# Performance work log

Hardware: AMD Instinct MI355X
Metric: run time of the kernel (lower is better)

The kernel has to match this reference:

```python
import jax, jax.numpy as jnp
import numpy as np

B, S, EMBED, HEADS = 2, 2048, 2048, 16
HEAD_DIM = EMBED // HEADS  # 128


def setup_inputs() -> dict:
    key = jax.random.key(0)
    k1, k2, k3 = jax.random.split(key, 3)
    x = jax.random.normal(k1, (B, S, EMBED), dtype=jnp.float32)
    # qkv_proj: Linear(EMBED -> 3*EMBED, bias=False); stored as [in, out]
    w_qkv = jax.random.normal(k2, (EMBED, 3 * EMBED), dtype=jnp.float32) / np.float32(np.sqrt(EMBED))
    # out_proj: Linear(EMBED -> EMBED, bias=False)
    w_out = jax.random.normal(k3, (EMBED, EMBED), dtype=jnp.float32) / np.float32(np.sqrt(EMBED))
    return {"x": x, "w_qkv": w_qkv, "w_out": w_out}


def reference(x, w_qkv, w_out):
    b, s, e = x.shape
    h, d = HEADS, e // HEADS
    qkv = x @ w_qkv                                  # [b, s, 3e]
    q, k, v = jnp.split(qkv, 3, axis=-1)             # each [b, s, e]
    q = q.reshape(b, s, h, d).transpose(0, 2, 1, 3)  # [b, h, s, d]
    k = k.reshape(b, s, h, d).transpose(0, 2, 1, 3)
    v = v.reshape(b, s, h, d).transpose(0, 2, 1, 3)
    scale = jnp.asarray(1.0 / np.sqrt(d), dtype=q.dtype)
    scores = jnp.einsum('bhqd,bhkd->bhqk', q, k) * scale  # [b, h, s, s]
    causal = jnp.tril(jnp.ones((s, s), dtype=bool))
    scores = jnp.where(causal, scores, -jnp.inf)
    attn = jax.nn.softmax(scores, axis=-1)
    ctx = jnp.einsum('bhqk,bhkd->bhqd', attn, v)     # [b, h, s, d]
    ctx = ctx.transpose(0, 2, 1, 3).reshape(b, s, e)
    return ctx @ w_out
```

## Files before the change

### kernel.cpp

```cpp
#include <hip/hip_runtime.h>
#include <cstdint>

#define S_LEN 2048
#define EMB   2048
#define NHEAD 16
#define HDIM  128
#define MROWS 4096
#define NQKV  6144

typedef __bf16 bf16x8 __attribute__((ext_vector_type(8)));
typedef __bf16 bf16x4 __attribute__((ext_vector_type(4)));
typedef float  f32x4  __attribute__((ext_vector_type(4)));

#define MFMA16(a, b, c) __builtin_amdgcn_mfma_f32_16x16x32_bf16((a), (b), (c), 0, 0, 0)

__device__ __forceinline__ unsigned short f2bf(float f) {
  unsigned u = __builtin_bit_cast(unsigned, f);
  u += 0x7fffu + ((u >> 16) & 1u);
  return (unsigned short)(u >> 16);
}
__device__ __forceinline__ float bf2f(unsigned short u) {
  unsigned v = ((unsigned)u) << 16;
  return __builtin_bit_cast(float, v);
}

__device__ __forceinline__ void gl_lds16(const unsigned short* g, unsigned short* l) {
  __builtin_amdgcn_global_load_lds(
      (const __attribute__((address_space(1))) void*)(uintptr_t)g,
      (__attribute__((address_space(3))) void*)(unsigned int)(uintptr_t)l,
      16, 0, 0);
}

__global__ void cast_bf16(const float* __restrict__ in, unsigned short* __restrict__ out, int n) {
  int i = (blockIdx.x * 256 + threadIdx.x) * 4;
  if (i >= n) return;
  float4 v = *(const float4*)(in + i);
  ushort4 o;
  o.x = f2bf(v.x); o.y = f2bf(v.y); o.z = f2bf(v.z); o.w = f2bf(v.w);
  *(ushort4*)(out + i) = o;
}

__global__ void transpose_cast(const float* __restrict__ in, unsigned short* __restrict__ out,
                               int R, int C) {
  __shared__ float tile[32][33];
  int bx = blockIdx.x << 5;
  int by = blockIdx.y << 5;
  int tx = threadIdx.x, ty = threadIdx.y;
  for (int j = 0; j < 32; j += 8)
    tile[ty + j][tx] = in[(size_t)(by + ty + j) * C + bx + tx];
  __syncthreads();
  for (int j = 0; j < 32; j += 8)
    out[(size_t)(bx + ty + j) * R + by + tx] = f2bf(tile[tx][ty + j]);
}

__global__ __launch_bounds__(512, 2) void gemm_qkv8(const unsigned short* __restrict__ A,
                                                    const unsigned short* __restrict__ Bt,
                                                    unsigned short* __restrict__ Qo,
                                                    unsigned short* __restrict__ Ko,
                                                    unsigned short* __restrict__ Vt) {
  extern __shared__ unsigned short lds[];
  unsigned short* Abuf = lds;
  unsigned short* Bbuf = lds + 32768;

  const int tid = threadIdx.x, w = tid >> 6, lane = tid & 63;
  const int fr = lane & 15, g = lane >> 4;
  const int gm = w >> 2, gn = w & 3;
  const int srow = tid >> 3, jp = tid & 7;

  const int bid = blockIdx.x;
  const int wg = (bid & 7) * 64 + (bid >> 3);
  const int mt = wg >> 5, nt = wg & 31;
  const int m0 = mt << 8;
  const int n0 = nt * 192;

  auto issueB = [&](int buf, int kk, int third) {
    const int row = (third << 6) + srow;
    gl_lds16(Bt + (size_t)(n0 + row) * 2048 + kk + ((jp ^ (row & 7)) << 3),
             Bbuf + buf * 12288 + (row << 6) + (jp << 3));
  };
  auto issueA = [&](int buf, int kk, int q) {
    const int row = (q << 6) + srow;
    gl_lds16(A + (size_t)(m0 + row) * 2048 + kk + ((jp ^ (row & 7)) << 3),
             Abuf + buf * 16384 + (row << 6) + (jp << 3));
  };

  f32x4 acc[8][3] = {};
  bf16x8 alo[4][2], ahi[4][2], bv[2][2], bc2[2];

  issueB(0, 0, 0); issueB(0, 0, 1); issueB(0, 0, 2);
  issueA(0, 0, 0); issueA(0, 0, 1); issueA(0, 0, 2); issueA(0, 0, 3);

  for (int t = 0; t < 32; ++t) {
    const int cb = t & 1, nb = cb ^ 1;
    const unsigned short* Ab = Abuf + cb * 16384;
    const unsigned short* Bb = Bbuf + cb * 12288;
    const int kn = (t + 1) << 6;

    asm volatile("s_waitcnt vmcnt(2)" ::: "memory");
    asm volatile("" ::: "memory");
    __builtin_amdgcn_s_barrier();
    asm volatile("" ::: "memory");
    if (t < 31) { issueB(nb, kn, 0); issueB(nb, kn, 1); issueB(nb, kn, 2); }
#pragma unroll
    for (int r = 0; r < 4; ++r)
#pragma unroll
      for (int ks = 0; ks < 2; ++ks)
        alo[r][ks] = *(const bf16x8*)(Ab + ((gm * 64 + r * 16 + fr) << 6) +
                                      ((((ks << 2) + g) ^ (fr & 7)) << 3));
#pragma unroll
    for (int c = 0; c < 2; ++c)
#pragma unroll
      for (int ks = 0; ks < 2; ++ks)
        bv[c][ks] = *(const bf16x8*)(Bb + ((gn * 48 + c * 16 + fr) << 6) +
                                     ((((ks << 2) + g) ^ (fr & 7)) << 3));
    __builtin_amdgcn_s_setprio(1);
#pragma unroll
    for (int ks = 0; ks < 2; ++ks)
#pragma unroll
      for (int r = 0; r < 4; ++r)
#pragma unroll
        for (int c = 0; c < 2; ++c)
          acc[r][c] = MFMA16(alo[r][ks], bv[c][ks], acc[r][c]);
    __builtin_amdgcn_s_setprio(0);

    if (t < 31) { asm volatile("s_waitcnt vmcnt(3)" ::: "memory"); }
    else        { asm volatile("s_waitcnt vmcnt(0)" ::: "memory"); }
    asm volatile("" ::: "memory");
    __builtin_amdgcn_s_barrier();
    asm volatile("" ::: "memory");
    if (t < 31) { issueA(nb, kn, 0); issueA(nb, kn, 1); }
#pragma unroll
    for (int ks = 0; ks < 2; ++ks)
      bc2[ks] = *(const bf16x8*)(Bb + ((gn * 48 + 32 + fr) << 6) +
                                 ((((ks << 2) + g) ^ (fr & 7)) << 3));
    __builtin_amdgcn_s_setprio(1);
#pragma unroll
    for (int ks = 0; ks < 2; ++ks)
#pragma unroll
      for (int r = 0; r < 4; ++r)
        acc[r][2] = MFMA16(alo[r][ks], bc2[ks], acc[r][2]);
    __builtin_amdgcn_s_setprio(0);
#pragma unroll
    for (int r = 0; r < 4; ++r)
#pragma unroll
      for (int ks = 0; ks < 2; ++ks)
        ahi[r][ks] = *(const bf16x8*)(Ab + ((128 + gm * 64 + r * 16 + fr) << 6) +
                                      ((((ks << 2) + g) ^ (fr & 7)) << 3));
    __builtin_amdgcn_s_setprio(1);
#pragma unroll
    for (int ks = 0; ks < 2; ++ks)
#pragma unroll
      for (int r = 0; r < 4; ++r)
        acc[4 + r][2] = MFMA16(ahi[r][ks], bc2[ks], acc[4 + r][2]);
    __builtin_amdgcn_s_setprio(0);

    asm volatile("" ::: "memory");
    __builtin_amdgcn_s_barrier();
    asm volatile("" ::: "memory");
    if (t < 31) { issueA(nb, kn, 2); issueA(nb, kn, 3); }
#pragma unroll
    for (int c = 0; c < 2; ++c)
#pragma unroll
      for (int ks = 0; ks < 2; ++ks)
        bv[c][ks] = *(const bf16x8*)(Bb + ((gn * 48 + c * 16 + fr) << 6) +
                                     ((((ks << 2) + g) ^ (fr & 7)) << 3));
    __builtin_amdgcn_s_setprio(1);
#pragma unroll
    for (int ks = 0; ks < 2; ++ks)
#pragma unroll
      for (int r = 0; r < 4; ++r)
#pragma unroll
        for (int c = 0; c < 2; ++c)
          acc[4 + r][c] = MFMA16(ahi[r][ks], bv[c][ks], acc[4 + r][c]);
    __builtin_amdgcn_s_setprio(0);
  }

  const int rowb = m0 & (S_LEN - 1);
  const int bbase = (m0 >> 11) * NHEAD;
  for (int r = 0; r < 8; ++r) {
    const int sl = rowb + ((r >> 2) << 7) + (gm << 6) + ((r & 3) << 4) + (g << 2);
    for (int c = 0; c < 3; ++c) {
      const int ncol = n0 + gn * 48 + c * 16;
      const int which = ncol >> 11;
      const int h = (ncol >> 7) & 15;
      const int d = (ncol & 127) + fr;
      const int bh = bbase + h;
      if (which == 2) {
        ushort4 pk;
        pk.x = f2bf(acc[r][c][0]); pk.y = f2bf(acc[r][c][1]);
        pk.z = f2bf(acc[r][c][2]); pk.w = f2bf(acc[r][c][3]);
        *(ushort4*)(Vt + ((size_t)bh * HDIM + d) * S_LEN + sl) = pk;
      } else {
        unsigned short* dst = which ? Ko : Qo;
        for (int q4 = 0; q4 < 4; ++q4)
          dst[((size_t)bh * S_LEN + sl + q4) * HDIM + d] = f2bf(acc[r][c][q4]);
      }
    }
  }
}

__global__ __launch_bounds__(256, 3) void attn(const unsigned short* __restrict__ Qg,
                                               const unsigned short* __restrict__ Kg,
                                               const unsigned short* __restrict__ Vtg,
                                               unsigned short* __restrict__ ctx,
                                               unsigned short* __restrict__ Opart,
                                               float* __restrict__ Lp) {
  __shared__ __align__(16) unsigned short SA[16384];
  __shared__ __align__(16) unsigned short Ps[8192];
  unsigned short* Qs = SA;
  unsigned short* Ks = SA;
  unsigned short* Vs = SA + 8192;

  const int blk = blockIdx.x;
  const int bh = blk & 31;
  const int t = blk >> 5;
  int qt, kt0, nkt, part;
  if (t < 8)       { qt = t;     kt0 = 0;  nkt = 2 * t + 2;       part = -1; }
  else if (t < 16) { qt = t;     kt0 = 0;  nkt = 16;              part = (bh << 3) + (qt - 8); }
  else             { qt = t - 8; kt0 = 16; nkt = 2 * qt - 14;     part = 256 + (bh << 3) + (qt - 8); }

  const int tid = threadIdx.x, wave = tid >> 6, lane = tid & 63;
  const int fr = lane & 15, g = lane >> 4;

  const unsigned short* qsrc = Qg + ((size_t)bh * S_LEN + (qt << 7)) * HDIM;
  for (int i = 0; i < 8; ++i) {
    int s0 = (i * 256 + tid) << 3;
    int q = s0 >> 7, jp = (s0 >> 3) & 15;
    gl_lds16(qsrc + (q << 7) + ((jp ^ (q & 15)) << 3), Qs + s0);
  }
  __builtin_amdgcn_s_waitcnt(0);
  __syncthreads();

  bf16x8 qf[2][4];
  for (int nbq = 0; nbq < 2; ++nbq)
    for (int kd = 0; kd < 4; ++kd) {
      int q = (wave << 5) + (nbq << 4) + fr;
      qf[nbq][kd] = *(const bf16x8*)(Qs + (q << 7) + ((((kd << 2) + g) ^ fr) << 3));
    }
  __syncthreads();

  float lsum[2] = {0.f, 0.f};
  f32x4 oacc[2][8] = {};
  const float scale = 0.08838834764831845f;

  const unsigned short* kbase = Kg + (size_t)bh * S_LEN * HDIM;
  const unsigned short* vbase = Vtg + (size_t)bh * HDIM * S_LEN;

  for (int kti = 0; kti < nkt; ++kti) {
    const int kt = kt0 + kti;
    const unsigned short* ks = kbase + ((size_t)kt << 6) * HDIM;
    const unsigned short* vs = vbase + (kt << 6);
    for (int i = 0; i < 4; ++i) {
      int s0 = (i * 256 + tid) << 3;
      int key = s0 >> 7, jk = (s0 >> 3) & 15;
      gl_lds16(ks + (key << 7) + ((jk ^ (key & 15)) << 3), Ks + s0);
      int d = s0 >> 6, jv = (s0 >> 3) & 7;
      gl_lds16(vs + (size_t)d * S_LEN + ((jv ^ (d & 7)) << 3), Vs + s0);
    }
    __builtin_amdgcn_s_waitcnt(0);
    __syncthreads();

    f32x4 sacc[2][4] = {};
    for (int kd = 0; kd < 4; ++kd)
      for (int kb = 0; kb < 4; ++kb) {
        bf16x8 kf = *(const bf16x8*)(Ks + (((kb << 4) + fr) << 7) + ((((kd << 2) + g) ^ fr) << 3));
        sacc[0][kb] = MFMA16(kf, qf[0][kd], sacc[0][kb]);
        sacc[1][kb] = MFMA16(kf, qf[1][kd], sacc[1][kb]);
      }

    const bool diag = (kt >= 2 * qt);
    for (int nbq = 0; nbq < 2; ++nbq) {
      const int qg = (qt << 7) + (wave << 5) + (nbq << 4) + fr;
      float sum = 0.f;
      for (int kb = 0; kb < 4; ++kb) {
        float p[4];
        for (int r = 0; r < 4; ++r) {
          float v = sacc[nbq][kb][r] * scale;
          if (diag) {
            int keyg = (kt << 6) + (kb << 4) + (g << 2) + r;
            if (keyg > qg) v = -__builtin_inff();
          }
          p[r] = __expf(v);
          sum += p[r];
        }
        ushort4 pk;
        pk.x = f2bf(p[0]); pk.y = f2bf(p[1]);
        pk.z = f2bf(p[2]); pk.w = f2bf(p[3]);
        *(ushort4*)(Ps + (((wave << 3) + (nbq << 2) + kb) << 8) + (lane << 2)) = pk;
      }
      lsum[nbq] += sum;
    }

    __builtin_amdgcn_s_waitcnt(0);

    for (int kc = 0; kc < 2; ++kc) {
      const int kbr = (kc << 1) + (g >> 1);
      bf16x8 ap[2];
      for (int h2 = 0; h2 < 2; ++h2) {
        const unsigned short* pb =
            Ps + (((wave << 3) + (h2 << 2) + kbr) << 8) + ((g & 1) << 7) + (fr << 2);
        bf16x4 a0 = *(const bf16x4*)pb;
        bf16x4 a1 = *(const bf16x4*)(pb + 64);
        bf16x8 a;
        a[0] = a0[0]; a[1] = a0[1]; a[2] = a0[2]; a[3] = a0[3];
        a[4] = a1[0]; a[5] = a1[1]; a[6] = a1[2]; a[7] = a1[3];
        ap[h2] = a;
      }
      for (int nd = 0; nd < 8; ++nd) {
        bf16x8 bv = *(const bf16x8*)(Vs + (((nd << 4) + fr) << 6) + ((((kc << 2) + g) ^ (fr & 7)) << 3));
        oacc[0][nd] = MFMA16(ap[0], bv, oacc[0][nd]);
        oacc[1][nd] = MFMA16(ap[1], bv, oacc[1][nd]);
      }
    }
    __syncthreads();
  }

  for (int nbq = 0; nbq < 2; ++nbq) {
    lsum[nbq] += __shfl_xor(lsum[nbq], 16);
    lsum[nbq] += __shfl_xor(lsum[nbq], 32);
  }

  if (part < 0) {
    const int b = bh >> 4, h = bh & 15;
    for (int mq = 0; mq < 2; ++mq)
      for (int r = 0; r < 4; ++r) {
        float lv = __shfl(lsum[mq], (lane & 48) | ((g << 2) + r));
        const float il = 1.0f / lv;
        const int s = (qt << 7) + (wave << 5) + (mq << 4) + (g << 2) + r;
        unsigned short* dst = ctx + ((size_t)(b * S_LEN + s) * EMB) + (h << 7);
        for (int nd = 0; nd < 8; ++nd)
          dst[(nd << 4) + fr] = f2bf(oacc[mq][nd][r] * il);
      }
  } else {
    unsigned short* Ob = Opart + ((size_t)part << 14);
    for (int mq = 0; mq < 2; ++mq)
      for (int r = 0; r < 4; ++r) {
        const int ql = (wave << 5) + (mq << 4) + (g << 2) + r;
        unsigned short* dst = Ob + (ql << 7);
        for (int nd = 0; nd < 8; ++nd)
          dst[(nd << 4) + fr] = f2bf(oacc[mq][nd][r]);
      }
    if (g == 0)
      for (int nbq = 0; nbq < 2; ++nbq) {
        const int ql = (wave << 5) + (nbq << 4) + fr;
        Lp[(part << 7) + ql] = lsum[nbq];
      }
  }
}

__global__ void attn_combine(const unsigned short* __restrict__ Op,
                             const float* __restrict__ Lp,
                             unsigned short* __restrict__ ctx) {
  const int tid = threadIdx.x;
  const int rid = blockIdx.x * 16 + (tid >> 4);
  const int l16 = tid & 15;
  const int bh = rid >> 10;
  const int qtl = (rid >> 7) & 7;
  const int ql = rid & 127;
  const int p = (bh << 3) + qtl;
  const float lA = Lp[(p << 7) + ql];
  const float lB = Lp[((256 + p) << 7) + ql];
  const float il = 1.0f / (lA + lB);
  const int d0 = l16 << 3;
  const unsigned short* a = Op + ((size_t)p << 14) + (ql << 7) + d0;
  const unsigned short* b = Op + ((size_t)(256 + p) << 14) + (ql << 7) + d0;
  const int bb = bh >> 4, h = bh & 15;
  const int s = ((qtl + 8) << 7) + ql;
  unsigned short* dst = ctx + ((size_t)(bb * S_LEN + s) * EMB) + (h << 7) + d0;
  ushort4 va0 = *(const ushort4*)a, va1 = *(const ushort4*)(a + 4);
  ushort4 vb0 = *(const ushort4*)b, vb1 = *(const ushort4*)(b + 4);
  ushort4 o0, o1;
  o0.x = f2bf((bf2f(va0.x) + bf2f(vb0.x)) * il);
  o0.y = f2bf((bf2f(va0.y) + bf2f(vb0.y)) * il);
  o0.z = f2bf((bf2f(va0.z) + bf2f(vb0.z)) * il);
  o0.w = f2bf((bf2f(va0.w) + bf2f(vb0.w)) * il);
  o1.x = f2bf((bf2f(va1.x) + bf2f(vb1.x)) * il);
  o1.y = f2bf((bf2f(va1.y) + bf2f(vb1.y)) * il);
  o1.z = f2bf((bf2f(va1.z) + bf2f(vb1.z)) * il);
  o1.w = f2bf((bf2f(va1.w) + bf2f(vb1.w)) * il);
  *(ushort4*)dst = o0;
  *(ushort4*)(dst + 4) = o1;
}

__global__ __launch_bounds__(256, 3) void gemm_out(const unsigned short* __restrict__ A,
                                                   const unsigned short* __restrict__ Bt,
                                                   float* __restrict__ C) {
  __shared__ __align__(16) unsigned short As[128 * 64];
  __shared__ __align__(16) unsigned short Bs[128 * 64];
  const int tid = threadIdx.x;
  const int n0 = blockIdx.x << 7;
  const int m0 = blockIdx.y << 7;
  const int wave = tid >> 6, lane = tid & 63;
  const int wm = (wave & 1) << 6, wn = (wave >> 1) << 6;
  const int fr = lane & 15, g = lane >> 4;
  const int q = tid >> 3;
  const int jp = tid & 7;
  f32x4 acc[4][4] = {};
  for (int k0 = 0; k0 < 2048; k0 += 64) {
    for (int i = 0; i < 4; ++i) {
      const int row = q + (i << 5);
      const int jsw = (jp ^ (row & 7)) << 3;
      gl_lds16(A + (size_t)(m0 + row) * 2048 + k0 + jsw, As + (row << 6) + (jp << 3));
      gl_lds16(Bt + (size_t)(n0 + row) * 2048 + k0 + jsw, Bs + (row << 6) + (jp << 3));
    }
    __builtin_amdgcn_s_waitcnt(0);
    __syncthreads();
    for (int ks = 0; ks < 2; ++ks) {
      const int slot = (((ks << 2) + g) ^ (fr & 7)) << 3;
      bf16x8 af[4], bfv[4];
      for (int i = 0; i < 4; ++i) af[i]  = *(const bf16x8*)(As + ((wm + (i << 4) + fr) << 6) + slot);
      for (int j = 0; j < 4; ++j) bfv[j] = *(const bf16x8*)(Bs + ((wn + (j << 4) + fr) << 6) + slot);
      for (int i = 0; i < 4; ++i)
        for (int j = 0; j < 4; ++j)
          acc[i][j] = MFMA16(af[i], bfv[j], acc[i][j]);
    }
    __syncthreads();
  }
  for (int i = 0; i < 4; ++i) {
    const int row = m0 + wm + (i << 4) + (g << 2);
    for (int j = 0; j < 4; ++j) {
      const int col = n0 + wn + (j << 4) + fr;
      for (int r = 0; r < 4; ++r)
        C[(size_t)(row + r) * EMB + col] = acc[i][j][r];
    }
  }
}

extern "C" void kernel_launch(void* const* d_in, const int* in_sizes, int n_in,
                              void* d_out, int out_size, void* d_ws, size_t ws_size,
                              hipStream_t stream) {
  const float* x    = (const float*)d_in[0];
  const float* wqkv = (const float*)d_in[1];
  const float* wout = (const float*)d_in[2];
  float* out = (float*)d_out;

  unsigned short* ws = (unsigned short*)d_ws;
  const size_t NELEM = (size_t)MROWS * EMB;
  unsigned short* xb    = ws;
  unsigned short* wqkvT = xb + NELEM;
  unsigned short* woutT = wqkvT + (size_t)NQKV * EMB;
  unsigned short* Q     = woutT + (size_t)EMB * EMB;
  unsigned short* K     = Q + NELEM;
  unsigned short* Vt    = K + NELEM;
  unsigned short* ctx   = xb;
  unsigned short* Opart = wqkvT;
  float* Lp = (float*)(Opart + ((size_t)512 << 14));

  static bool attr_done = false;
  if (!attr_done) {
    (void)hipFuncSetAttribute((const void*)gemm_qkv8,
                              hipFuncAttributeMaxDynamicSharedMemorySize, 114688);
    attr_done = true;
  }

  cast_bf16<<<8192, 256, 0, stream>>>(x, xb, (int)NELEM);
  transpose_cast<<<dim3(NQKV / 32, EMB / 32), dim3(32, 8), 0, stream>>>(wqkv, wqkvT, EMB, NQKV);
  transpose_cast<<<dim3(EMB / 32, EMB / 32), dim3(32, 8), 0, stream>>>(wout, woutT, EMB, EMB);
  gemm_qkv8<<<512, 512, 114688, stream>>>(xb, wqkvT, Q, K, Vt);
  attn<<<768, 256, 0, stream>>>(Q, K, Vt, ctx, Opart, Lp);
  attn_combine<<<2048, 256, 0, stream>>>(Opart, Lp, ctx);
  gemm_out<<<dim3(EMB / 128, MROWS / 128), 256, 0, stream>>>(ctx, woutT, out);
}
```

Measured before the change: 365.1 us.

## Share a templated pipelined GEMM core between the QKV and output projections

```diff
diff --git a/kernel.cpp b/kernel.cpp
--- a/kernel.cpp
+++ b/kernel.cpp
@@ -30,6 +30,9 @@
       (__attribute__((address_space(3))) void*)(unsigned int)(uintptr_t)l,
       16, 0, 0);
 }
+
+#define FENCE() asm volatile("" ::: "memory")
+#define BARRIER() do { FENCE(); __builtin_amdgcn_s_barrier(); FENCE(); } while (0)
 
 __global__ void cast_bf16(const float* __restrict__ in, unsigned short* __restrict__ out, int n) {
   int i = (blockIdx.x * 256 + threadIdx.x) * 4;
@@ -53,134 +56,160 @@
     out[(size_t)(bx + ty + j) * R + by + tx] = f2bf(tile[tx][ty + j]);
 }
 
-__global__ __launch_bounds__(512, 2) void gemm_qkv8(const unsigned short* __restrict__ A,
+template<int NCOL>
+__device__ __forceinline__ void gemm_pipe2(const unsigned short* __restrict__ Ap,
+                                           const unsigned short* __restrict__ Bp,
+                                           int m0, int n0, f32x4 (&acc)[8][NCOL]) {
+  constexpr int BN = 128 * NCOL;
+  constexpr int BISS = 2 * NCOL;
+  constexpr int NT = 32;
+  extern __shared__ unsigned short lds[];
+  unsigned short* Abuf = lds;
+  unsigned short* Bbuf = lds + 16384;
+
+  const int tid = threadIdx.x, w = tid >> 6, lane = tid & 63;
+  const int fr = lane & 15, g = lane >> 4;
+  const int srow = tid >> 3, jp = tid & 7;
+
+  auto issueA = [&](int buf, int kk, int idx) {
+    const int row = (idx << 6) + srow;
+    gl_lds16(Ap + (size_t)(m0 + row) * 2048 + kk + ((jp ^ (row & 7)) << 3),
+             Abuf + (buf << 13) + (row << 6) + (jp << 3));
+  };
+  auto issueB = [&](int buf, int kk, int idx) {
+    const int row = (idx << 6) + srow;
+    gl_lds16(Bp + (size_t)(n0 + row) * 2048 + kk + ((jp ^ (row & 7)) << 3),
+             Bbuf + buf * (BN * 64) + (row << 6) + (jp << 3));
+  };
+
+#pragma unroll
+  for (int i = 0; i < BISS; ++i) issueB(0, 0, i);
+  issueA(0, 0, 0); issueA(0, 0, 1);
+  issueB(1, 64, 0); issueB(1, 64, 1);
+  asm volatile("s_waitcnt vmcnt(2)" ::: "memory");
+  __builtin_amdgcn_s_barrier();
+  FENCE();
+
+  bf16x8 bfr[NCOL][2];
+  for (int t = 0; t < NT; ++t) {
+    const int cb = t & 1, nb = cb ^ 1;
+    const unsigned short* Ab = Abuf + (cb << 13);
+    const unsigned short* Bb = Bbuf + cb * (BN * 64);
+    const int kn = (t + 1) << 6;
+    const bool s1 = (t + 1 < NT), s2 = (t + 2 < NT);
+
+    bf16x8 af[2][2];
+#pragma unroll
+    for (int c = 0; c < NCOL; ++c)
+#pragma unroll
+      for (int ks = 0; ks < 2; ++ks)
+        bfr[c][ks] = *(const bf16x8*)(Bb + ((w * 16 * NCOL + c * 16 + fr) << 6) +
+                                      ((((ks << 2) + g) ^ (fr & 7)) << 3));
+#pragma unroll
+    for (int rr = 0; rr < 2; ++rr)
+#pragma unroll
+      for (int ks = 0; ks < 2; ++ks)
+        af[rr][ks] = *(const bf16x8*)(Ab + (((rr * 16) + fr) << 6) +
+                                      ((((ks << 2) + g) ^ (fr & 7)) << 3));
+    if (s1) {
+      issueB(nb, kn, 2); issueB(nb, kn, 3);
+      if (NCOL == 3) issueB(nb, kn, 4);
+    }
+    BARRIER();
+    __builtin_amdgcn_s_setprio(1);
+#pragma unroll
+    for (int ks = 0; ks < 2; ++ks)
+#pragma unroll
+      for (int rr = 0; rr < 2; ++rr)
+#pragma unroll
+        for (int c = 0; c < NCOL; ++c)
+          acc[rr][c] = MFMA16(af[rr][ks], bfr[c][ks], acc[rr][c]);
+    __builtin_amdgcn_s_setprio(0);
+
+#pragma unroll
+    for (int rr = 0; rr < 2; ++rr)
+#pragma unroll
+      for (int ks = 0; ks < 2; ++ks)
+        af[rr][ks] = *(const bf16x8*)(Ab + (((32 + rr * 16) + fr) << 6) +
+                                      ((((ks << 2) + g) ^ (fr & 7)) << 3));
+    if (s1) {
+      if (NCOL == 3) issueB(nb, kn, 5);
+      issueA(nb, kn, 0); issueA(nb, kn, 1);
+    }
+    BARRIER();
+    __builtin_amdgcn_s_setprio(1);
+#pragma unroll
+    for (int ks = 0; ks < 2; ++ks)
+#pragma unroll
+      for (int rr = 0; rr < 2; ++rr)
+#pragma unroll
+        for (int c = 0; c < NCOL; ++c)
+          acc[2 + rr][c] = MFMA16(af[rr][ks], bfr[c][ks], acc[2 + rr][c]);
+    __builtin_amdgcn_s_setprio(0);
+
+#pragma unroll
+    for (int rr = 0; rr < 2; ++rr)
+#pragma unroll
+      for (int ks = 0; ks < 2; ++ks)
+        af[rr][ks] = *(const bf16x8*)(Ab + (((64 + rr * 16) + fr) << 6) +
+                                      ((((ks << 2) + g) ^ (fr & 7)) << 3));
+    BARRIER();
+    __builtin_amdgcn_s_setprio(1);
+#pragma unroll
+    for (int ks = 0; ks < 2; ++ks)
+#pragma unroll
+      for (int rr = 0; rr < 2; ++rr)
+#pragma unroll
+        for (int c = 0; c < NCOL; ++c)
+          acc[4 + rr][c] = MFMA16(af[rr][ks], bfr[c][ks], acc[4 + rr][c]);
+    __builtin_amdgcn_s_setprio(0);
+
+#pragma unroll
+    for (int rr = 0; rr < 2; ++rr)
+#pragma unroll
+      for (int ks = 0; ks < 2; ++ks)
+        af[rr][ks] = *(const bf16x8*)(Ab + (((96 + rr * 16) + fr) << 6) +
+                                      ((((ks << 2) + g) ^ (fr & 7)) << 3));
+    if (s2) {
+      const int kn2 = (t + 2) << 6;
+      issueB(cb, kn2, 0); issueB(cb, kn2, 1);
+      asm volatile("s_waitcnt vmcnt(2)" ::: "memory");
+    } else if (s1) {
+      asm volatile("s_waitcnt vmcnt(0)" ::: "memory");
+    }
+    BARRIER();
+    __builtin_amdgcn_s_setprio(1);
+#pragma unroll
+    for (int ks = 0; ks < 2; ++ks)
+#pragma unroll
+      for (int rr = 0; rr < 2; ++rr)
+#pragma unroll
+        for (int c = 0; c < NCOL; ++c)
+          acc[6 + rr][c] = MFMA16(af[rr][ks], bfr[c][ks], acc[6 + rr][c]);
+    __builtin_amdgcn_s_setprio(0);
+  }
+}
+
+__global__ __launch_bounds__(512, 2) void gemm_qkv9(const unsigned short* __restrict__ A,
                                                     const unsigned short* __restrict__ Bt,
                                                     unsigned short* __restrict__ Qo,
                                                     unsigned short* __restrict__ Ko,
                                                     unsigned short* __restrict__ Vt) {
-  extern __shared__ unsigned short lds[];
-  unsigned short* Abuf = lds;
-  unsigned short* Bbuf = lds + 32768;
+  const int bid = blockIdx.x;
+  const int wg = (bid & 7) * 64 + (bid >> 3);
+  const int mt = wg & 31, nt = wg >> 5;
+  const int m0 = mt << 7, n0 = nt * 384;
+  f32x4 acc[8][3] = {};
+  gemm_pipe2<3>(A, Bt, m0, n0, acc);
 
   const int tid = threadIdx.x, w = tid >> 6, lane = tid & 63;
   const int fr = lane & 15, g = lane >> 4;
-  const int gm = w >> 2, gn = w & 3;
-  const int srow = tid >> 3, jp = tid & 7;
-
-  const int bid = blockIdx.x;
-  const int wg = (bid & 7) * 64 + (bid >> 3);
-  const int mt = wg >> 5, nt = wg & 31;
-  const int m0 = mt << 8;
-  const int n0 = nt * 192;
-
-  auto issueB = [&](int buf, int kk, int third) {
-    const int row = (third << 6) + srow;
-    gl_lds16(Bt + (size_t)(n0 + row) * 2048 + kk + ((jp ^ (row & 7)) << 3),
-             Bbuf + buf * 12288 + (row << 6) + (jp << 3));
-  };
-  auto issueA = [&](int buf, int kk, int q) {
-    const int row = (q << 6) + srow;
-    gl_lds16(A + (size_t)(m0 + row) * 2048 + kk + ((jp ^ (row & 7)) << 3),
-             Abuf + buf * 16384 + (row << 6) + (jp << 3));
-  };
-
-  f32x4 acc[8][3] = {};
-  bf16x8 alo[4][2], ahi[4][2], bv[2][2], bc2[2];
-
-  issueB(0, 0, 0); issueB(0, 0, 1); issueB(0, 0, 2);
-  issueA(0, 0, 0); issueA(0, 0, 1); issueA(0, 0, 2); issueA(0, 0, 3);
-
-  for (int t = 0; t < 32; ++t) {
-    const int cb = t & 1, nb = cb ^ 1;
-    const unsigned short* Ab = Abuf + cb * 16384;
-    const unsigned short* Bb = Bbuf + cb * 12288;
-    const int kn = (t + 1) << 6;
-
-    asm volatile("s_waitcnt vmcnt(2)" ::: "memory");
-    asm volatile("" ::: "memory");
-    __builtin_amdgcn_s_barrier();
-    asm volatile("" ::: "memory");
-    if (t < 31) { issueB(nb, kn, 0); issueB(nb, kn, 1); issueB(nb, kn, 2); }
-#pragma unroll
-    for (int r = 0; r < 4; ++r)
-#pragma unroll
-      for (int ks = 0; ks < 2; ++ks)
-        alo[r][ks] = *(const bf16x8*)(Ab + ((gm * 64 + r * 16 + fr) << 6) +
-                                      ((((ks << 2) + g) ^ (fr & 7)) << 3));
-#pragma unroll
-    for (int c = 0; c < 2; ++c)
-#pragma unroll
-      for (int ks = 0; ks < 2; ++ks)
-        bv[c][ks] = *(const bf16x8*)(Bb + ((gn * 48 + c * 16 + fr) << 6) +
-                                     ((((ks << 2) + g) ^ (fr & 7)) << 3));
-    __builtin_amdgcn_s_setprio(1);
-#pragma unroll
-    for (int ks = 0; ks < 2; ++ks)
-#pragma unroll
-      for (int r = 0; r < 4; ++r)
-#pragma unroll
-        for (int c = 0; c < 2; ++c)
-          acc[r][c] = MFMA16(alo[r][ks], bv[c][ks], acc[r][c]);
-    __builtin_amdgcn_s_setprio(0);
-
-    if (t < 31) { asm volatile("s_waitcnt vmcnt(3)" ::: "memory"); }
-    else        { asm volatile("s_waitcnt vmcnt(0)" ::: "memory"); }
-    asm volatile("" ::: "memory");
-    __builtin_amdgcn_s_barrier();
-    asm volatile("" ::: "memory");
-    if (t < 31) { issueA(nb, kn, 0); issueA(nb, kn, 1); }
-#pragma unroll
-    for (int ks = 0; ks < 2; ++ks)
-      bc2[ks] = *(const bf16x8*)(Bb + ((gn * 48 + 32 + fr) << 6) +
-                                 ((((ks << 2) + g) ^ (fr & 7)) << 3));
-    __builtin_amdgcn_s_setprio(1);
-#pragma unroll
-    for (int ks = 0; ks < 2; ++ks)
-#pragma unroll
-      for (int r = 0; r < 4; ++r)
-        acc[r][2] = MFMA16(alo[r][ks], bc2[ks], acc[r][2]);
-    __builtin_amdgcn_s_setprio(0);
-#pragma unroll
-    for (int r = 0; r < 4; ++r)
-#pragma unroll
-      for (int ks = 0; ks < 2; ++ks)
-        ahi[r][ks] = *(const bf16x8*)(Ab + ((128 + gm * 64 + r * 16 + fr) << 6) +
-                                      ((((ks << 2) + g) ^ (fr & 7)) << 3));
-    __builtin_amdgcn_s_setprio(1);
-#pragma unroll
-    for (int ks = 0; ks < 2; ++ks)
-#pragma unroll
-      for (int r = 0; r < 4; ++r)
-        acc[4 + r][2] = MFMA16(ahi[r][ks], bc2[ks], acc[4 + r][2]);
-    __builtin_amdgcn_s_setprio(0);
-
-    asm volatile("" ::: "memory");
-    __builtin_amdgcn_s_barrier();
-    asm volatile("" ::: "memory");
-    if (t < 31) { issueA(nb, kn, 2); issueA(nb, kn, 3); }
-#pragma unroll
-    for (int c = 0; c < 2; ++c)
-#pragma unroll
-      for (int ks = 0; ks < 2; ++ks)
-        bv[c][ks] = *(const bf16x8*)(Bb + ((gn * 48 + c * 16 + fr) << 6) +
-                                     ((((ks << 2) + g) ^ (fr & 7)) << 3));
-    __builtin_amdgcn_s_setprio(1);
-#pragma unroll
-    for (int ks = 0; ks < 2; ++ks)
-#pragma unroll
-      for (int r = 0; r < 4; ++r)
-#pragma unroll
-        for (int c = 0; c < 2; ++c)
-          acc[4 + r][c] = MFMA16(ahi[r][ks], bv[c][ks], acc[4 + r][c]);
-    __builtin_amdgcn_s_setprio(0);
-  }
-
   const int rowb = m0 & (S_LEN - 1);
   const int bbase = (m0 >> 11) * NHEAD;
   for (int r = 0; r < 8; ++r) {
-    const int sl = rowb + ((r >> 2) << 7) + (gm << 6) + ((r & 3) << 4) + (g << 2);
+    const int sl = rowb + r * 16 + (g << 2);
     for (int c = 0; c < 3; ++c) {
-      const int ncol = n0 + gn * 48 + c * 16;
+      const int ncol = n0 + w * 48 + c * 16;
       const int which = ncol >> 11;
       const int h = (ncol >> 7) & 15;
       const int d = (ncol & 127) + fr;
@@ -195,6 +224,28 @@
         for (int q4 = 0; q4 < 4; ++q4)
           dst[((size_t)bh * S_LEN + sl + q4) * HDIM + d] = f2bf(acc[r][c][q4]);
       }
+    }
+  }
+}
+
+__global__ __launch_bounds__(512, 2) void gemm_out9(const unsigned short* __restrict__ A,
+                                                    const unsigned short* __restrict__ Bt,
+                                                    float* __restrict__ C) {
+  const int bid = blockIdx.x;
+  const int wg = (bid & 7) * 32 + (bid >> 3);
+  const int mt = wg & 31, nt = wg >> 5;
+  const int m0 = mt << 7, n0 = nt << 8;
+  f32x4 acc[8][2] = {};
+  gemm_pipe2<2>(A, Bt, m0, n0, acc);
+
+  const int tid = threadIdx.x, w = tid >> 6, lane = tid & 63;
+  const int fr = lane & 15, g = lane >> 4;
+  for (int r = 0; r < 8; ++r) {
+    const int row = m0 + r * 16 + (g << 2);
+    for (int c = 0; c < 2; ++c) {
+      const int col = n0 + w * 32 + c * 16 + fr;
+      for (int q4 = 0; q4 < 4; ++q4)
+        C[(size_t)(row + q4) * EMB + col] = acc[r][c][q4];
     }
   }
 }
@@ -382,50 +433,6 @@
   *(ushort4*)(dst + 4) = o1;
 }
 
-__global__ __launch_bounds__(256, 3) void gemm_out(const unsigned short* __restrict__ A,
-                                                   const unsigned short* __restrict__ Bt,
-                                                   float* __restrict__ C) {
-  __shared__ __align__(16) unsigned short As[128 * 64];
-  __shared__ __align__(16) unsigned short Bs[128 * 64];
-  const int tid = threadIdx.x;
-  const int n0 = blockIdx.x << 7;
-  const int m0 = blockIdx.y << 7;
-  const int wave = tid >> 6, lane = tid & 63;
-  const int wm = (wave & 1) << 6, wn = (wave >> 1) << 6;
-  const int fr = lane & 15, g = lane >> 4;
-  const int q = tid >> 3;
-  const int jp = tid & 7;
-  f32x4 acc[4][4] = {};
-  for (int k0 = 0; k0 < 2048; k0 += 64) {
-    for (int i = 0; i < 4; ++i) {
-      const int row = q + (i << 5);
-      const int jsw = (jp ^ (row & 7)) << 3;
-      gl_lds16(A + (size_t)(m0 + row) * 2048 + k0 + jsw, As + (row << 6) + (jp << 3));
-      gl_lds16(Bt + (size_t)(n0 + row) * 2048 + k0 + jsw, Bs + (row << 6) + (jp << 3));
-    }
-    __builtin_amdgcn_s_waitcnt(0);
-    __syncthreads();
-    for (int ks = 0; ks < 2; ++ks) {
-      const int slot = (((ks << 2) + g) ^ (fr & 7)) << 3;
-      bf16x8 af[4], bfv[4];
-      for (int i = 0; i < 4; ++i) af[i]  = *(const bf16x8*)(As + ((wm + (i << 4) + fr) << 6) + slot);
-      for (int j = 0; j < 4; ++j) bfv[j] = *(const bf16x8*)(Bs + ((wn + (j << 4) + fr) << 6) + slot);
-      for (int i = 0; i < 4; ++i)
-        for (int j = 0; j < 4; ++j)
-          acc[i][j] = MFMA16(af[i], bfv[j], acc[i][j]);
-    }
-    __syncthreads();
-  }
-  for (int i = 0; i < 4; ++i) {
-    const int row = m0 + wm + (i << 4) + (g << 2);
-    for (int j = 0; j < 4; ++j) {
-      const int col = n0 + wn + (j << 4) + fr;
-      for (int r = 0; r < 4; ++r)
-        C[(size_t)(row + r) * EMB + col] = acc[i][j][r];
-    }
-  }
-}
-
 extern "C" void kernel_launch(void* const* d_in, const int* in_sizes, int n_in,
                               void* d_out, int out_size, void* d_ws, size_t ws_size,
                               hipStream_t stream) {
@@ -448,16 +455,18 @@
 
   static bool attr_done = false;
   if (!attr_done) {
-    (void)hipFuncSetAttribute((const void*)gemm_qkv8,
-                              hipFuncAttributeMaxDynamicSharedMemorySize, 114688);
+    (void)hipFuncSetAttribute((const void*)gemm_qkv9,
+                              hipFuncAttributeMaxDynamicSharedMemorySize, 131072);
+    (void)hipFuncSetAttribute((const void*)gemm_out9,
+                              hipFuncAttributeMaxDynamicSharedMemorySize, 98304);
     attr_done = true;
   }
 
   cast_bf16<<<8192, 256, 0, stream>>>(x, xb, (int)NELEM);
   transpose_cast<<<dim3(NQKV / 32, EMB / 32), dim3(32, 8), 0, stream>>>(wqkv, wqkvT, EMB, NQKV);
   transpose_cast<<<dim3(EMB / 32, EMB / 32), dim3(32, 8), 0, stream>>>(wout, woutT, EMB, EMB);
-  gemm_qkv8<<<512, 512, 114688, stream>>>(xb, wqkvT, Q, K, Vt);
+  gemm_qkv9<<<512, 512, 131072, stream>>>(xb, wqkvT, Q, K, Vt);
   attn<<<768, 256, 0, stream>>>(Q, K, Vt, ctx, Opart, Lp);
   attn_combine<<<2048, 256, 0, stream>>>(Opart, Lp, ctx);
-  gemm_out<<<dim3(EMB / 128, MROWS / 128), 256, 0, stream>>>(ctx, woutT, out);
-}
+  gemm_out9<<<256, 512, 98304, stream>>>(ctx, woutT, out);
+}
```

Result: no change. 362.6 us (-0.7%).
